# Optimization experiments

Measured on AMD Instinct MI355X. Metric: run time of the kernel, lower is better.

Reference implementation:

```python
import jax, jax.numpy as jnp
import numpy as np

N = 50000    # nodes
E = 600000   # edges
F = 128      # num_features
ED = 16      # edge_dim
H = 4        # heads
D = 32       # per-head channels = hidden_units // heads
HID = H * D  # hidden_units = 128
C = 10       # num_classes


def _lin(k, fan_in, fan_out):
    # torch.nn.Linear-style init scale
    return jax.random.uniform(k, (fan_in, fan_out), jnp.float32, -1.0, 1.0) / np.sqrt(fan_in)


def setup_inputs() -> dict:
    key = jax.random.key(0)
    ks = jax.random.split(key, 24)
    inp = {
        "x": jax.random.normal(ks[0], (N, F), jnp.float32),
        "edge_index": jax.random.randint(ks[1], (2, E), 0, N, dtype=jnp.int32),
        "edge_attr": jax.random.normal(ks[2], (E, ED), jnp.float32),
    }
    j = 3
    for l, ind in enumerate([F, HID]):
        specs = {"q": (ind, HID, True), "k": (ind, HID, True), "v": (ind, HID, True),
                 "e": (ED, HID, False), "s": (ind, HID, True)}
        for nm, (i, o, bias) in specs.items():
            inp[f"W{nm}{l}"] = _lin(ks[j], i, o); j += 1
            if bias:
                inp[f"b{nm}{l}"] = jnp.zeros((o,), jnp.float32)
    inp["Wout"] = _lin(ks[j], HID, C)
    inp["bout"] = jnp.zeros((C,), jnp.float32)
    return inp


def _transformer_conv(x, src, dst, eattr, Wq, bq, Wk, bk, Wv, bv, We, Ws, bs):
    # PyG TransformerConv: concat=True, root_weight=True, beta=False, eval dropout.
    n = x.shape[0]
    q = (x @ Wq + bq).reshape(n, H, D)
    k = (x @ Wk + bk).reshape(n, H, D)
    v = (x @ Wv + bv).reshape(n, H, D)
    e = (eattr @ We).reshape(-1, H, D)           # edge embedding, added to key and value
    kj = k[src] + e                              # [E, H, D]
    vj = v[src] + e                              # [E, H, D]
    logits = jnp.einsum("ehd,ehd->eh", q[dst], kj) / np.sqrt(D)
    m = jax.ops.segment_max(logits, dst, num_segments=n)          # [N, H]
    ex = jnp.exp(logits - m[dst])
    denom = jax.ops.segment_sum(ex, dst, num_segments=n)          # [N, H]
    alpha = ex / (denom[dst] + 1e-16)                             # PyG softmax eps
    out = jax.ops.segment_sum(vj * alpha[..., None], dst, num_segments=n)
    return out.reshape(n, HID) + x @ Ws + bs                      # concat heads + skip


def reference(x, edge_index, edge_attr,
              Wq0, bq0, Wk0, bk0, Wv0, bv0, We0, Ws0, bs0,
              Wq1, bq1, Wk1, bk1, Wv1, bv1, We1, Ws1, bs1,
              Wout, bout):
    src, dst = edge_index[0], edge_index[1]
    h = jax.nn.relu(_transformer_conv(x, src, dst, edge_attr,
                                      Wq0, bq0, Wk0, bk0, Wv0, bv0, We0, Ws0, bs0))
    h = jax.nn.relu(_transformer_conv(h, src, dst, edge_attr,
                                      Wq1, bq1, Wk1, bk1, Wv1, bv1, We1, Ws1, bs1))
    logits = h @ Wout + bout
    return jax.nn.log_softmax(logits, axis=1)
```

## Files before the change

### kernel.cpp

```cpp
#include <hip/hip_runtime.h>

typedef unsigned short u16;
typedef __attribute__((ext_vector_type(4))) u16 u16x4;
typedef __attribute__((ext_vector_type(8))) u16 u16x8;
typedef __attribute__((ext_vector_type(8))) short short8;
typedef __attribute__((ext_vector_type(4))) float f32x4;
typedef __attribute__((ext_vector_type(4))) float f4;

#define NN 50000
#define NE 600000
#define HEADS 4
#define DH 32
#define HIDU 128
#define NC 10
#define NBLK 196

__device__ __forceinline__ float bf2f(u16 u) {
    union { unsigned int i; float f; } c; c.i = ((unsigned int)u) << 16; return c.f;
}
__device__ __forceinline__ u16 f2bf(float f) {
    union { float f; unsigned int i; } c; c.f = f;
    unsigned int x = c.i;
    return (u16)((x + 0x7fffu + ((x >> 16) & 1u)) >> 16);
}

__global__ void k_zero(int* p, int n) {
    int i = blockIdx.x * blockDim.x + threadIdx.x;
    if (i < n) p[i] = 0;
}

__global__ void k_hist(const int* __restrict__ dst, int* __restrict__ deg) {
    int i = blockIdx.x * blockDim.x + threadIdx.x;
    if (i < NE) atomicAdd(&deg[dst[i]], 1);
}

__global__ __launch_bounds__(256) void scan_a(const int* __restrict__ deg,
                                              int* __restrict__ bsum) {
    __shared__ int red[4];
    int i = blockIdx.x * 256 + threadIdx.x;
    int v = (i < NN) ? deg[i] : 0;
    #pragma unroll
    for (int off = 1; off < 64; off <<= 1) v += __shfl_xor(v, off);
    if ((threadIdx.x & 63) == 0) red[threadIdx.x >> 6] = v;
    __syncthreads();
    if (threadIdx.x == 0) bsum[blockIdx.x] = red[0] + red[1] + red[2] + red[3];
}

__global__ __launch_bounds__(256) void scan_b(const int* __restrict__ bsum,
                                              int* __restrict__ boff,
                                              int* __restrict__ row_ptr) {
    __shared__ int s[256];
    int t = threadIdx.x;
    int v = (t < NBLK) ? bsum[t] : 0;
    s[t] = v;
    __syncthreads();
    for (int off = 1; off < 256; off <<= 1) {
        int x = (t >= off) ? s[t - off] : 0;
        __syncthreads();
        s[t] += x;
        __syncthreads();
    }
    if (t < NBLK) boff[t] = s[t] - v;
    if (t == 0) row_ptr[NN] = NE;
}

__global__ __launch_bounds__(256) void scan_c(const int* __restrict__ deg,
                                              const int* __restrict__ boff,
                                              int* __restrict__ row_ptr,
                                              int* __restrict__ cursor) {
    __shared__ int s[256];
    int t = threadIdx.x;
    int i = blockIdx.x * 256 + t;
    int v = (i < NN) ? deg[i] : 0;
    s[t] = v;
    __syncthreads();
    for (int off = 1; off < 256; off <<= 1) {
        int x = (t >= off) ? s[t - off] : 0;
        __syncthreads();
        s[t] += x;
        __syncthreads();
    }
    if (i < NN) {
        int r = boff[blockIdx.x] + s[t] - v;
        row_ptr[i] = r;
        cursor[i] = r;
    }
}

__global__ void k_scatter(const int* __restrict__ ei, const float* __restrict__ eattr,
                          int* __restrict__ cursor,
                          int* __restrict__ csr_src, u16* __restrict__ ea16) {
    int i = blockIdx.x * blockDim.x + threadIdx.x;
    if (i < NE) {
        int s = ei[i];
        int d = ei[NE + i];
        int pos = atomicAdd(&cursor[d], 1);
        csr_src[pos] = s;
        const f4* ep = (const f4*)(eattr + (size_t)i * 16);
        f4 a = ep[0], b = ep[1], c = ep[2], dd = ep[3];
        u16x8 o0, o1;
        #pragma unroll
        for (int j = 0; j < 4; j++) {
            o0[j] = f2bf(a[j]); o0[4 + j] = f2bf(b[j]);
            o1[j] = f2bf(c[j]); o1[4 + j] = f2bf(dd[j]);
        }
        *(u16x8*)(ea16 + (size_t)pos * 16)     = o0;
        *(u16x8*)(ea16 + (size_t)pos * 16 + 8) = o1;
    }
}

__global__ __launch_bounds__(256) void k_cvt(const float* __restrict__ in,
                                             u16* __restrict__ hi, u16* __restrict__ lo) {
    int i = blockIdx.x * 256 + threadIdx.x;
    const f4* p = (const f4*)(in + (size_t)i * 8);
    f4 a = p[0], b = p[1];
    float v[8] = {a[0], a[1], a[2], a[3], b[0], b[1], b[2], b[3]};
    u16x8 h, l;
    #pragma unroll
    for (int j = 0; j < 8; j++) {
        u16 hh = f2bf(v[j]);
        float r = v[j] - bf2f(hh);
        h[j] = hh; l[j] = f2bf(r);
    }
    *(u16x8*)(hi + (size_t)i * 8) = h;
    *(u16x8*)(lo + (size_t)i * 8) = l;
}

__global__ void k_cvtw(const float* w0, const float* w1, const float* w2, const float* w3,
                       const float* w4, const float* w5, const float* w6, const float* w7,
                       u16* __restrict__ hi, u16* __restrict__ lo) {
    const float* w;
    switch (blockIdx.x) {
        case 0: w = w0; break; case 1: w = w1; break;
        case 2: w = w2; break; case 3: w = w3; break;
        case 4: w = w4; break; case 5: w = w5; break;
        case 6: w = w6; break; default: w = w7; break;
    }
    u16* oh = hi + blockIdx.x * 16384;
    u16* ol = lo + blockIdx.x * 16384;
    for (int i = 0; i < 64; i++) {
        int idx = threadIdx.x + i * 256;
        int k = idx >> 7, n = idx & 127;
        float v = w[idx];
        u16 h = f2bf(v);
        float r = v - bf2f(h);
        oh[n * 128 + k] = h;
        ol[n * 128 + k] = f2bf(r);
    }
}

__global__ __launch_bounds__(256) void gemm_qkv(
    const u16* __restrict__ Xhi, const u16* __restrict__ WtHi,
    const float* __restrict__ b0, const float* __restrict__ b1,
    const float* __restrict__ b2,
    float* __restrict__ outq, u16* __restrict__ outk, u16* __restrict__ outv,
    int nrows)
{
    __shared__ u16 Bs[128 * 128];
    const int mat = blockIdx.y;
    const u16* wh = WtHi + mat * 16384;

    #pragma unroll
    for (int i = 0; i < 8; i++) {
        int idx = threadIdx.x + i * 256;
        int n = idx >> 4, g = idx & 15;
        Bs[0] = Bs[0];
        *(u16x8*)(&Bs[n * 128 + ((g ^ (n & 15)) << 3)]) = *(const u16x8*)(wh + n * 128 + g * 8);
    }
    __syncthreads();

    const int wave = threadIdx.x >> 6, lane = threadIdx.x & 63;
    const int n0 = lane & 15;
    const int qw = lane >> 4;
    const int kq = qw * 8;

    const u16* xh[2];
    #pragma unroll
    for (int rt = 0; rt < 2; rt++) {
        int arow = blockIdx.x * 128 + wave * 32 + rt * 16 + n0;
        int arow_c = arow < nrows ? arow : nrows - 1;
        xh[rt] = Xhi + (size_t)arow_c * HIDU + kq;
    }

    f32x4 acc[2][8];
    #pragma unroll
    for (int rt = 0; rt < 2; rt++)
        #pragma unroll
        for (int nt = 0; nt < 8; nt++) acc[rt][nt] = (f32x4){0.f, 0.f, 0.f, 0.f};

    #pragma unroll
    for (int ks = 0; ks < 4; ks++) {
        short8 ah[2];
        #pragma unroll
        for (int rt = 0; rt < 2; rt++) ah[rt] = *(const short8*)(xh[rt] + ks * 32);
        #pragma unroll
        for (int nt = 0; nt < 8; nt++) {
            const int boff = (nt * 16 + n0) * 128 + (((ks << 2) + qw) ^ n0) * 8;
            short8 bh = *(const short8*)(&Bs[boff]);
            #pragma unroll
            for (int rt = 0; rt < 2; rt++)
                acc[rt][nt] = __builtin_amdgcn_mfma_f32_16x16x32_bf16(ah[rt], bh, acc[rt][nt], 0, 0, 0);
        }
    }

    const float* bia = (mat == 0) ? b0 : (mat == 1) ? b1 : b2;
    #pragma unroll
    for (int rt = 0; rt < 2; rt++) {
        const int rbase = blockIdx.x * 128 + wave * 32 + rt * 16 + qw * 4;
        #pragma unroll
        for (int nt = 0; nt < 8; nt++) {
            int col = nt * 16 + n0;
            float bv = bia[col];
            #pragma unroll
            for (int r = 0; r < 4; r++) {
                int grow = rbase + r;
                if (grow < nrows) {
                    float v = acc[rt][nt][r] + bv;
                    if (mat == 0)      outq[(size_t)grow * HIDU + col] = v;
                    else if (mat == 1) outk[(size_t)grow * HIDU + col] = f2bf(v);
                    else               outv[(size_t)grow * HIDU + col] = f2bf(v);
                }
            }
        }
    }
}

__global__ __launch_bounds__(256) void gemm_s(
    const u16* __restrict__ Xhi, const u16* __restrict__ Xlo,
    const u16* __restrict__ wh, const u16* __restrict__ wl,
    const float* __restrict__ bia, float* __restrict__ outs, int nrows)
{
    __shared__ u16 Bs[2 * 128 * 128];

    #pragma unroll
    for (int i = 0; i < 8; i++) {
        int idx = threadIdx.x + i * 256;
        int n = idx >> 4, g = idx & 15;
        int dst = n * 128 + ((g ^ (n & 15)) << 3);
        *(u16x8*)(&Bs[dst])         = *(const u16x8*)(wh + n * 128 + g * 8);
        *(u16x8*)(&Bs[16384 + dst]) = *(const u16x8*)(wl + n * 128 + g * 8);
    }
    __syncthreads();

    const int wave = threadIdx.x >> 6, lane = threadIdx.x & 63;
    const int n0 = lane & 15;
    const int qw = lane >> 4;
    const int kq = qw * 8;

    const u16* xh[2]; const u16* xl[2];
    #pragma unroll
    for (int rt = 0; rt < 2; rt++) {
        int arow = blockIdx.x * 128 + wave * 32 + rt * 16 + n0;
        int arow_c = arow < nrows ? arow : nrows - 1;
        xh[rt] = Xhi + (size_t)arow_c * HIDU + kq;
        xl[rt] = Xlo + (size_t)arow_c * HIDU + kq;
    }

    f32x4 acc[2][8];
    #pragma unroll
    for (int rt = 0; rt < 2; rt++)
        #pragma unroll
        for (int nt = 0; nt < 8; nt++) acc[rt][nt] = (f32x4){0.f, 0.f, 0.f, 0.f};

    #pragma unroll
    for (int ks = 0; ks < 4; ks++) {
        short8 ah[2], al[2];
        #pragma unroll
        for (int rt = 0; rt < 2; rt++) {
            ah[rt] = *(const short8*)(xh[rt] + ks * 32);
            al[rt] = *(const short8*)(xl[rt] + ks * 32);
        }
        #pragma unroll
        for (int nt = 0; nt < 8; nt++) {
            const int boff = (nt * 16 + n0) * 128 + (((ks << 2) + qw) ^ n0) * 8;
            short8 bh = *(const short8*)(&Bs[boff]);
            short8 bl = *(const short8*)(&Bs[16384 + boff]);
            #pragma unroll
            for (int rt = 0; rt < 2; rt++) {
                acc[rt][nt] = __builtin_amdgcn_mfma_f32_16x16x32_bf16(ah[rt], bh, acc[rt][nt], 0, 0, 0);
                acc[rt][nt] = __builtin_amdgcn_mfma_f32_16x16x32_bf16(al[rt], bh, acc[rt][nt], 0, 0, 0);
                acc[rt][nt] = __builtin_amdgcn_mfma_f32_16x16x32_bf16(ah[rt], bl, acc[rt][nt], 0, 0, 0);
            }
        }
    }

    #pragma unroll
    for (int rt = 0; rt < 2; rt++) {
        const int rbase = blockIdx.x * 128 + wave * 32 + rt * 16 + qw * 4;
        #pragma unroll
        for (int nt = 0; nt < 8; nt++) {
            int col = nt * 16 + n0;
            float bv = bia[col];
            #pragma unroll
            for (int r = 0; r < 4; r++) {
                int grow = rbase + r;
                if (grow < nrows) outs[(size_t)grow * HIDU + col] = acc[rt][nt][r] + bv;
            }
        }
    }
}

__global__ __launch_bounds__(256) void attn(
    const float* __restrict__ qb, const u16* __restrict__ kb, const u16* __restrict__ vb,
    const float* __restrict__ sb, const u16* __restrict__ ea16, const float* __restrict__ We,
    const int* __restrict__ row_ptr, const int* __restrict__ csr_src,
    float* __restrict__ hout_f32, u16* __restrict__ hout_hi, u16* __restrict__ hout_lo,
    int mode)
{
    __shared__ float WeS[4 * 513];
    #pragma unroll
    for (int i = 0; i < 8; i++) {
        int idx = threadIdx.x + i * 256;
        int tt = idx >> 7, c = idx & 127;
        int h = c >> 5, j = c & 31;
        WeS[h * 513 + tt * 32 + j] = We[idx];
    }
    __syncthreads();

    int gtid = blockIdx.x * 256 + threadIdx.x;
    int n   = gtid >> 4;
    int l16 = gtid & 15;
    int h   = l16 >> 2;
    int sub = l16 & 3;
    const int lane = threadIdx.x & 63;
    const float* WeH = &WeS[h * 513];
    const int j0  = sub * 8;
    const int ch0 = h * DH + j0;
    const int t0  = sub * 4;

    float qreg[8];
    float g4[4];
    {
        const f4* qp = (const f4*)(qb + (size_t)n * HIDU + h * DH);
        float q32[32];
        #pragma unroll
        for (int c = 0; c < 8; c++) {
            f4 x = qp[c];
            #pragma unroll
            for (int j = 0; j < 4; j++) q32[c * 4 + j] = x[j];
        }
        #pragma unroll
        for (int tt = 0; tt < 4; tt++) {
            float a = 0.f;
            #pragma unroll
            for (int j = 0; j < 32; j++) a += q32[j] * WeH[(t0 + tt) * 32 + j];
            g4[tt] = a;
        }
        #pragma unroll
        for (int j = 0; j < 8; j++) qreg[j] = q32[j0 + j];
    }

    float m = -INFINITY, l = 0.f;
    float O[8];
    float a4[4];
    #pragma unroll
    for (int j = 0; j < 8; j++) O[j] = 0.f;
    #pragma unroll
    for (int tt = 0; tt < 4; tt++) a4[tt] = 0.f;

    const int r0 = row_ptr[n], r1 = row_ptr[n + 1];
    const float inv = 0.17677669529663687f;

    for (int e = r0; e < r1; e += 2) {
        bool has2 = (e + 1 < r1);
        int e1i = has2 ? e + 1 : e;
        int s0 = csr_src[e];
        int s1 = csr_src[e1i];
        u16x4 e0 = *(const u16x4*)(ea16 + (size_t)e * 16 + t0);
        u16x4 e1 = *(const u16x4*)(ea16 + (size_t)e1i * 16 + t0);

        u16x8 k0 = *(const u16x8*)(kb + (size_t)s0 * HIDU + ch0);
        u16x8 v0 = *(const u16x8*)(vb + (size_t)s0 * HIDU + ch0);
        u16x8 k1 = *(const u16x8*)(kb + (size_t)s1 * HIDU + ch0);
        u16x8 v1 = *(const u16x8*)(vb + (size_t)s1 * HIDU + ch0);

        float ea0[4], ea1[4];
        #pragma unroll
        for (int tt = 0; tt < 4; tt++) { ea0[tt] = bf2f(e0[tt]); ea1[tt] = bf2f(e1[tt]); }

        float d0 = 0.f, d1 = 0.f;
        #pragma unroll
        for (int j = 0; j < 8; j++) {
            d0 += qreg[j] * bf2f(k0[j]);
            d1 += qreg[j] * bf2f(k1[j]);
        }
        #pragma unroll
        for (int tt = 0; tt < 4; tt++) {
            d0 += g4[tt] * ea0[tt];
            d1 += g4[tt] * ea1[tt];
        }
        d0 += __shfl_xor(d0, 1);  d1 += __shfl_xor(d1, 1);
        d0 += __shfl_xor(d0, 2);  d1 += __shfl_xor(d1, 2);

        float logit0 = d0 * inv;
        float logit1 = has2 ? d1 * inv : -INFINITY;
        float mn = fmaxf(m, fmaxf(logit0, logit1));
        float corr = __expf(m - mn);
        float w0 = __expf(logit0 - mn);
        float w1 = __expf(logit1 - mn);
        l = l * corr + w0 + w1;
        #pragma unroll
        for (int j = 0; j < 8; j++)
            O[j] = O[j] * corr + w0 * bf2f(v0[j]) + w1 * bf2f(v1[j]);
        #pragma unroll
        for (int tt = 0; tt < 4; tt++)
            a4[tt] = a4[tt] * corr + w0 * ea0[tt] + w1 * ea1[tt];
        m = mn;
    }

    float af[16];
    #pragma unroll
    for (int t = 0; t < 16; t++)
        af[t] = __shfl(a4[t & 3], (lane & ~3) | (t >> 2));

    float invl = 1.0f / (l + 1e-16f);
    const float* sp = sb + (size_t)n * HIDU + ch0;
    const size_t obase = (size_t)n * HIDU + ch0;

    float vals[8];
    #pragma unroll
    for (int j = 0; j < 8; j++) {
        float ev = 0.f;
        #pragma unroll
        for (int t = 0; t < 16; t++) ev += af[t] * WeH[t * 32 + j0 + j];
        vals[j] = fmaxf((O[j] + ev) * invl + sp[j], 0.f);
    }
    if (mode == 0) {
        u16x8 hh, ll;
        #pragma unroll
        for (int j = 0; j < 8; j++) {
            u16 hv = f2bf(vals[j]);
            hh[j] = hv;
            ll[j] = f2bf(vals[j] - bf2f(hv));
        }
        *(u16x8*)(hout_hi + obase) = hh;
        *(u16x8*)(hout_lo + obase) = ll;
    } else {
        f4 r0v, r1v;
        #pragma unroll
        for (int j = 0; j < 4; j++) { r0v[j] = vals[j]; r1v[j] = vals[4 + j]; }
        *(f4*)(hout_f32 + obase) = r0v;
        *(f4*)(hout_f32 + obase + 4) = r1v;
    }
}

__global__ __launch_bounds__(256) void head_out(
    const float* __restrict__ hb, const float* __restrict__ Wout, const float* __restrict__ bout,
    float* __restrict__ out, int nnodes)
{
    __shared__ float Ws[HIDU * NC];
    __shared__ float bs[NC];
    for (int i = 0; i < 5; i++) {
        int idx = threadIdx.x + i * 256;
        if (idx < HIDU * NC) Ws[idx] = Wout[idx];
    }
    if (threadIdx.x < NC) bs[threadIdx.x] = bout[threadIdx.x];
    __syncthreads();

    int n = blockIdx.x * 256 + threadIdx.x;
    if (n >= nnodes) return;

    float lg[NC];
    #pragma unroll
    for (int c = 0; c < NC; c++) lg[c] = bs[c];
    const f4* hp = (const f4*)(hb + (size_t)n * HIDU);
    #pragma unroll
    for (int kc = 0; kc < 32; kc++) {
        f4 hv = hp[kc];
        #pragma unroll
        for (int j = 0; j < 4; j++) {
            float h = hv[j];
            int kk = kc * 4 + j;
            #pragma unroll
            for (int c = 0; c < NC; c++) lg[c] += h * Ws[kk * NC + c];
        }
    }
    float mx = lg[0];
    #pragma unroll
    for (int c = 1; c < NC; c++) mx = fmaxf(mx, lg[c]);
    float sum = 0.f;
    #pragma unroll
    for (int c = 0; c < NC; c++) sum += __expf(lg[c] - mx);
    float lse = mx + __logf(sum);
    #pragma unroll
    for (int c = 0; c < NC; c++) out[(size_t)n * NC + c] = lg[c] - lse;
}

extern "C" void kernel_launch(void* const* d_in, const int* in_sizes, int n_in,
                              void* d_out, int out_size, void* d_ws, size_t ws_size,
                              hipStream_t stream) {
    const float* x     = (const float*)d_in[0];
    const int*   ei    = (const int*)d_in[1];
    const float* eattr = (const float*)d_in[2];
    const float *Wq0 = (const float*)d_in[3],  *bq0 = (const float*)d_in[4];
    const float *Wk0 = (const float*)d_in[5],  *bk0 = (const float*)d_in[6];
    const float *Wv0 = (const float*)d_in[7],  *bv0 = (const float*)d_in[8];
    const float *We0 = (const float*)d_in[9];
    const float *Ws0 = (const float*)d_in[10], *bs0 = (const float*)d_in[11];
    const float *Wq1 = (const float*)d_in[12], *bq1 = (const float*)d_in[13];
    const float *Wk1 = (const float*)d_in[14], *bk1 = (const float*)d_in[15];
    const float *Wv1 = (const float*)d_in[16], *bv1 = (const float*)d_in[17];
    const float *We1 = (const float*)d_in[18];
    const float *Ws1 = (const float*)d_in[19], *bs1 = (const float*)d_in[20];
    const float *Wout = (const float*)d_in[21], *bout = (const float*)d_in[22];

    char* p = (char*)d_ws;
    auto alloc = [&](size_t bytes) -> void* {
        void* r = (void*)p;
        p += (bytes + 255) & ~(size_t)255;
        return r;
    };
    int* deg      = (int*)alloc(NN * 4);
    int* row_ptr  = (int*)alloc((NN + 1) * 4);
    int* cursor   = (int*)alloc(NN * 4);
    int* bsum     = (int*)alloc(NBLK * 4);
    int* boff     = (int*)alloc(NBLK * 4);
    int* csr_src  = (int*)alloc((size_t)NE * 4);
    float* qb     = (float*)alloc((size_t)NN * HIDU * 4);
    u16* kb       = (u16*)alloc((size_t)NN * HIDU * 2);
    u16* vb       = (u16*)alloc((size_t)NN * HIDU * 2);
    float* sbuf   = (float*)alloc((size_t)NN * HIDU * 4);
    float* hbuf   = (float*)alloc((size_t)NN * HIDU * 4);
    u16* ea16     = (u16*)alloc((size_t)NE * 16 * 2);
    u16* xhi      = (u16*)alloc((size_t)NN * HIDU * 2);
    u16* xlo      = (u16*)alloc((size_t)NN * HIDU * 2);
    u16* wthi     = (u16*)alloc(8 * 16384 * 2);
    u16* wtlo     = (u16*)alloc(8 * 16384 * 2);

    k_zero<<<(NN + 255) / 256, 256, 0, stream>>>(deg, NN);
    k_hist<<<(NE + 255) / 256, 256, 0, stream>>>(ei + NE, deg);
    scan_a<<<NBLK, 256, 0, stream>>>(deg, bsum);
    scan_b<<<1, 256, 0, stream>>>(bsum, boff, row_ptr);
    scan_c<<<NBLK, 256, 0, stream>>>(deg, boff, row_ptr, cursor);
    k_scatter<<<(NE + 255) / 256, 256, 0, stream>>>(ei, eattr, cursor, csr_src, ea16);

    k_cvtw<<<8, 256, 0, stream>>>(Wq0, Wk0, Wv0, Ws0, Wq1, Wk1, Wv1, Ws1, wthi, wtlo);

    const int gcv = (NN * HIDU / 8 + 255) / 256;
    const int gm = (NN + 127) / 128;
    const int ga = (NN * 16) / 256;

    k_cvt<<<gcv, 256, 0, stream>>>(x, xhi, xlo);
    gemm_qkv<<<dim3(gm, 3), 256, 0, stream>>>(xhi, wthi, bq0, bk0, bv0, qb, kb, vb, NN);
    gemm_s<<<gm, 256, 0, stream>>>(xhi, xlo, wthi + 3 * 16384, wtlo + 3 * 16384, bs0, sbuf, NN);
    attn<<<ga, 256, 0, stream>>>(qb, kb, vb, sbuf, ea16, We0,
                                 row_ptr, csr_src, hbuf, xhi, xlo, 0);
    gemm_qkv<<<dim3(gm, 3), 256, 0, stream>>>(xhi, wthi + 4 * 16384, bq1, bk1, bv1, qb, kb, vb, NN);
    gemm_s<<<gm, 256, 0, stream>>>(xhi, xlo, wthi + 7 * 16384, wtlo + 7 * 16384, bs1, sbuf, NN);
    attn<<<ga, 256, 0, stream>>>(qb, kb, vb, sbuf, ea16, We1,
                                 row_ptr, csr_src, hbuf, (u16*)nullptr, (u16*)nullptr, 1);
    head_out<<<(NN + 255) / 256, 256, 0, stream>>>(hbuf, Wout, bout, (float*)d_out, NN);
}
```

Measured before the change: 489.8 us.

## Fuse bf16 split into GEMMs, fuse output head into attention, use DPP reductions

Removes the standalone x-to-bf16 hi/lo conversion kernel and the bf16 hi/lo writes from layer-0 attention. The GEMMs now read fp32 activations directly and split them in registers, with the hi part taken by truncation instead of rounding. The separate head_out kernel is folded into layer-1 attention, which computes the 10-class logits and log-softmax per node through shared memory. Shuffle-xor reductions are replaced with DPP quad permutes. This saves launches and intermediate traffic, but the GEMMs read twice as many A bytes, truncation changes precision slightly, and attention gains more shared memory and a serial per-lane output dot product.

```diff
diff --git a/kernel.cpp b/kernel.cpp
--- a/kernel.cpp
+++ b/kernel.cpp
@@ -22,6 +22,14 @@
     union { float f; unsigned int i; } c; c.f = f;
     unsigned int x = c.i;
     return (u16)((x + 0x7fffu + ((x >> 16) & 1u)) >> 16);
+}
+__device__ __forceinline__ float qadd_xor1(float v) {
+    int o = __builtin_amdgcn_update_dpp(0, __float_as_int(v), 0xB1, 0xF, 0xF, true);
+    return v + __int_as_float(o);
+}
+__device__ __forceinline__ float qadd_xor2(float v) {
+    int o = __builtin_amdgcn_update_dpp(0, __float_as_int(v), 0x4E, 0xF, 0xF, true);
+    return v + __int_as_float(o);
 }
 
 __global__ void k_zero(int* p, int n) {
@@ -109,23 +117,6 @@
     }
 }
 
-__global__ __launch_bounds__(256) void k_cvt(const float* __restrict__ in,
-                                             u16* __restrict__ hi, u16* __restrict__ lo) {
-    int i = blockIdx.x * 256 + threadIdx.x;
-    const f4* p = (const f4*)(in + (size_t)i * 8);
-    f4 a = p[0], b = p[1];
-    float v[8] = {a[0], a[1], a[2], a[3], b[0], b[1], b[2], b[3]};
-    u16x8 h, l;
-    #pragma unroll
-    for (int j = 0; j < 8; j++) {
-        u16 hh = f2bf(v[j]);
-        float r = v[j] - bf2f(hh);
-        h[j] = hh; l[j] = f2bf(r);
-    }
-    *(u16x8*)(hi + (size_t)i * 8) = h;
-    *(u16x8*)(lo + (size_t)i * 8) = l;
-}
-
 __global__ void k_cvtw(const float* w0, const float* w1, const float* w2, const float* w3,
                        const float* w4, const float* w5, const float* w6, const float* w7,
                        u16* __restrict__ hi, u16* __restrict__ lo) {
@@ -150,7 +141,7 @@
 }
 
 __global__ __launch_bounds__(256) void gemm_qkv(
-    const u16* __restrict__ Xhi, const u16* __restrict__ WtHi,
+    const float* __restrict__ X, const u16* __restrict__ WtHi,
     const float* __restrict__ b0, const float* __restrict__ b1,
     const float* __restrict__ b2,
     float* __restrict__ outq, u16* __restrict__ outk, u16* __restrict__ outv,
@@ -164,7 +155,6 @@
     for (int i = 0; i < 8; i++) {
         int idx = threadIdx.x + i * 256;
         int n = idx >> 4, g = idx & 15;
-        Bs[0] = Bs[0];
         *(u16x8*)(&Bs[n * 128 + ((g ^ (n & 15)) << 3)]) = *(const u16x8*)(wh + n * 128 + g * 8);
     }
     __syncthreads();
@@ -174,12 +164,12 @@
     const int qw = lane >> 4;
     const int kq = qw * 8;
 
-    const u16* xh[2];
+    const float* xp[2];
     #pragma unroll
     for (int rt = 0; rt < 2; rt++) {
         int arow = blockIdx.x * 128 + wave * 32 + rt * 16 + n0;
         int arow_c = arow < nrows ? arow : nrows - 1;
-        xh[rt] = Xhi + (size_t)arow_c * HIDU + kq;
+        xp[rt] = X + (size_t)arow_c * HIDU + kq;
     }
 
     f32x4 acc[2][8];
@@ -192,7 +182,15 @@
     for (int ks = 0; ks < 4; ks++) {
         short8 ah[2];
         #pragma unroll
-        for (int rt = 0; rt < 2; rt++) ah[rt] = *(const short8*)(xh[rt] + ks * 32);
+        for (int rt = 0; rt < 2; rt++) {
+            f4 a0 = *(const f4*)(xp[rt] + ks * 32);
+            f4 a1 = *(const f4*)(xp[rt] + ks * 32 + 4);
+            #pragma unroll
+            for (int j = 0; j < 4; j++) {
+                ah[rt][j]     = (short)(__float_as_uint(a0[j]) >> 16);
+                ah[rt][4 + j] = (short)(__float_as_uint(a1[j]) >> 16);
+            }
+        }
         #pragma unroll
         for (int nt = 0; nt < 8; nt++) {
             const int boff = (nt * 16 + n0) * 128 + (((ks << 2) + qw) ^ n0) * 8;
@@ -226,7 +224,7 @@
 }
 
 __global__ __launch_bounds__(256) void gemm_s(
-    const u16* __restrict__ Xhi, const u16* __restrict__ Xlo,
+    const float* __restrict__ X,
     const u16* __restrict__ wh, const u16* __restrict__ wl,
     const float* __restrict__ bia, float* __restrict__ outs, int nrows)
 {
@@ -247,13 +245,12 @@
     const int qw = lane >> 4;
     const int kq = qw * 8;
 
-    const u16* xh[2]; const u16* xl[2];
+    const float* xp[2];
     #pragma unroll
     for (int rt = 0; rt < 2; rt++) {
         int arow = blockIdx.x * 128 + wave * 32 + rt * 16 + n0;
         int arow_c = arow < nrows ? arow : nrows - 1;
-        xh[rt] = Xhi + (size_t)arow_c * HIDU + kq;
-        xl[rt] = Xlo + (size_t)arow_c * HIDU + kq;
+        xp[rt] = X + (size_t)arow_c * HIDU + kq;
     }
 
     f32x4 acc[2][8];
@@ -267,8 +264,19 @@
         short8 ah[2], al[2];
         #pragma unroll
         for (int rt = 0; rt < 2; rt++) {
-            ah[rt] = *(const short8*)(xh[rt] + ks * 32);
-            al[rt] = *(const short8*)(xl[rt] + ks * 32);
+            f4 a0 = *(const f4*)(xp[rt] + ks * 32);
+            f4 a1 = *(const f4*)(xp[rt] + ks * 32 + 4);
+            #pragma unroll
+            for (int j = 0; j < 4; j++) {
+                unsigned u0 = __float_as_uint(a0[j]);
+                unsigned u1 = __float_as_uint(a1[j]);
+                ah[rt][j]     = (short)(u0 >> 16);
+                ah[rt][4 + j] = (short)(u1 >> 16);
+                float r0 = a0[j] - __uint_as_float(u0 & 0xffff0000u);
+                float r1 = a1[j] - __uint_as_float(u1 & 0xffff0000u);
+                al[rt][j]     = (short)(__float_as_uint(r0) >> 16);
+                al[rt][4 + j] = (short)(__float_as_uint(r1) >> 16);
+            }
         }
         #pragma unroll
         for (int nt = 0; nt < 8; nt++) {
@@ -304,16 +312,29 @@
     const float* __restrict__ qb, const u16* __restrict__ kb, const u16* __restrict__ vb,
     const float* __restrict__ sb, const u16* __restrict__ ea16, const float* __restrict__ We,
     const int* __restrict__ row_ptr, const int* __restrict__ csr_src,
-    float* __restrict__ hout_f32, u16* __restrict__ hout_hi, u16* __restrict__ hout_lo,
-    int mode)
+    float* __restrict__ hout_f32,
+    const float* __restrict__ Wout, const float* __restrict__ bout,
+    float* __restrict__ out_logits, int mode)
 {
     __shared__ float WeS[4 * 513];
+    __shared__ float WoS[HIDU * NC];
+    __shared__ float boS[NC];
+    __shared__ float hrowS[16 * 132];
+    __shared__ float lgS[16 * 16];
+
     #pragma unroll
     for (int i = 0; i < 8; i++) {
         int idx = threadIdx.x + i * 256;
         int tt = idx >> 7, c = idx & 127;
         int h = c >> 5, j = c & 31;
         WeS[h * 513 + tt * 32 + j] = We[idx];
+    }
+    if (mode == 1) {
+        for (int i = 0; i < 5; i++) {
+            int idx = threadIdx.x + i * 256;
+            if (idx < HIDU * NC) WoS[idx] = Wout[idx];
+        }
+        if (threadIdx.x < NC) boS[threadIdx.x] = bout[threadIdx.x];
     }
     __syncthreads();
 
@@ -389,8 +410,8 @@
             d0 += g4[tt] * ea0[tt];
             d1 += g4[tt] * ea1[tt];
         }
-        d0 += __shfl_xor(d0, 1);  d1 += __shfl_xor(d1, 1);
-        d0 += __shfl_xor(d0, 2);  d1 += __shfl_xor(d1, 2);
+        d0 = qadd_xor1(d0);  d1 = qadd_xor1(d1);
+        d0 = qadd_xor2(d0);  d1 = qadd_xor2(d1);
 
         float logit0 = d0 * inv;
         float logit1 = has2 ? d1 * inv : -INFINITY;
@@ -415,7 +436,6 @@
 
     float invl = 1.0f / (l + 1e-16f);
     const float* sp = sb + (size_t)n * HIDU + ch0;
-    const size_t obase = (size_t)n * HIDU + ch0;
 
     float vals[8];
     #pragma unroll
@@ -425,65 +445,43 @@
         for (int t = 0; t < 16; t++) ev += af[t] * WeH[t * 32 + j0 + j];
         vals[j] = fmaxf((O[j] + ev) * invl + sp[j], 0.f);
     }
+
     if (mode == 0) {
-        u16x8 hh, ll;
-        #pragma unroll
-        for (int j = 0; j < 8; j++) {
-            u16 hv = f2bf(vals[j]);
-            hh[j] = hv;
-            ll[j] = f2bf(vals[j] - bf2f(hv));
-        }
-        *(u16x8*)(hout_hi + obase) = hh;
-        *(u16x8*)(hout_lo + obase) = ll;
-    } else {
+        const size_t obase = (size_t)n * HIDU + ch0;
         f4 r0v, r1v;
         #pragma unroll
         for (int j = 0; j < 4; j++) { r0v[j] = vals[j]; r1v[j] = vals[4 + j]; }
         *(f4*)(hout_f32 + obase) = r0v;
         *(f4*)(hout_f32 + obase + 4) = r1v;
-    }
-}
-
-__global__ __launch_bounds__(256) void head_out(
-    const float* __restrict__ hb, const float* __restrict__ Wout, const float* __restrict__ bout,
-    float* __restrict__ out, int nnodes)
-{
-    __shared__ float Ws[HIDU * NC];
-    __shared__ float bs[NC];
-    for (int i = 0; i < 5; i++) {
-        int idx = threadIdx.x + i * 256;
-        if (idx < HIDU * NC) Ws[idx] = Wout[idx];
-    }
-    if (threadIdx.x < NC) bs[threadIdx.x] = bout[threadIdx.x];
-    __syncthreads();
-
-    int n = blockIdx.x * 256 + threadIdx.x;
-    if (n >= nnodes) return;
-
-    float lg[NC];
-    #pragma unroll
-    for (int c = 0; c < NC; c++) lg[c] = bs[c];
-    const f4* hp = (const f4*)(hb + (size_t)n * HIDU);
-    #pragma unroll
-    for (int kc = 0; kc < 32; kc++) {
-        f4 hv = hp[kc];
-        #pragma unroll
-        for (int j = 0; j < 4; j++) {
-            float h = hv[j];
-            int kk = kc * 4 + j;
-            #pragma unroll
-            for (int c = 0; c < NC; c++) lg[c] += h * Ws[kk * NC + c];
-        }
-    }
-    float mx = lg[0];
-    #pragma unroll
-    for (int c = 1; c < NC; c++) mx = fmaxf(mx, lg[c]);
-    float sum = 0.f;
-    #pragma unroll
-    for (int c = 0; c < NC; c++) sum += __expf(lg[c] - mx);
-    float lse = mx + __logf(sum);
-    #pragma unroll
-    for (int c = 0; c < NC; c++) out[(size_t)n * NC + c] = lg[c] - lse;
+    } else {
+        const int cb = threadIdx.x >> 4;
+        float* hr = &hrowS[cb * 132];
+        f4 w0v, w1v;
+        #pragma unroll
+        for (int j = 0; j < 4; j++) { w0v[j] = vals[j]; w1v[j] = vals[4 + j]; }
+        *(f4*)(hr + ch0) = w0v;
+        *(f4*)(hr + ch0 + 4) = w1v;
+        if (l16 < NC) {
+            float lg = boS[l16];
+            for (int ch = 0; ch < HIDU; ch += 4) {
+                f4 hv = *(const f4*)(hr + ch);
+                #pragma unroll
+                for (int j = 0; j < 4; j++) lg += hv[j] * WoS[(ch + j) * NC + l16];
+            }
+            lgS[cb * 16 + l16] = lg;
+        }
+        if (l16 < NC) {
+            float lgc = lgS[cb * 16 + l16];
+            float mx = -INFINITY;
+            #pragma unroll
+            for (int c = 0; c < NC; c++) mx = fmaxf(mx, lgS[cb * 16 + c]);
+            float sum = 0.f;
+            #pragma unroll
+            for (int c = 0; c < NC; c++) sum += __expf(lgS[cb * 16 + c] - mx);
+            float lse = mx + __logf(sum);
+            out_logits[(size_t)n * NC + l16] = lgc - lse;
+        }
+    }
 }
 
 extern "C" void kernel_launch(void* const* d_in, const int* in_sizes, int n_in,
@@ -522,8 +520,6 @@
     float* sbuf   = (float*)alloc((size_t)NN * HIDU * 4);
     float* hbuf   = (float*)alloc((size_t)NN * HIDU * 4);
     u16* ea16     = (u16*)alloc((size_t)NE * 16 * 2);
-    u16* xhi      = (u16*)alloc((size_t)NN * HIDU * 2);
-    u16* xlo      = (u16*)alloc((size_t)NN * HIDU * 2);
     u16* wthi     = (u16*)alloc(8 * 16384 * 2);
     u16* wtlo     = (u16*)alloc(8 * 16384 * 2);
 
@@ -536,18 +532,15 @@
 
     k_cvtw<<<8, 256, 0, stream>>>(Wq0, Wk0, Wv0, Ws0, Wq1, Wk1, Wv1, Ws1, wthi, wtlo);
 
-    const int gcv = (NN * HIDU / 8 + 255) / 256;
     const int gm = (NN + 127) / 128;
     const int ga = (NN * 16) / 256;
 
-    k_cvt<<<gcv, 256, 0, stream>>>(x, xhi, xlo);
-    gemm_qkv<<<dim3(gm, 3), 256, 0, stream>>>(xhi, wthi, bq0, bk0, bv0, qb, kb, vb, NN);
-    gemm_s<<<gm, 256, 0, stream>>>(xhi, xlo, wthi + 3 * 16384, wtlo + 3 * 16384, bs0, sbuf, NN);
-    attn<<<ga, 256, 0, stream>>>(qb, kb, vb, sbuf, ea16, We0,
-                                 row_ptr, csr_src, hbuf, xhi, xlo, 0);
-    gemm_qkv<<<dim3(gm, 3), 256, 0, stream>>>(xhi, wthi + 4 * 16384, bq1, bk1, bv1, qb, kb, vb, NN);
-    gemm_s<<<gm, 256, 0, stream>>>(xhi, xlo, wthi + 7 * 16384, wtlo + 7 * 16384, bs1, sbuf, NN);
-    attn<<<ga, 256, 0, stream>>>(qb, kb, vb, sbuf, ea16, We1,
-                                 row_ptr, csr_src, hbuf, (u16*)nullptr, (u16*)nullptr, 1);
-    head_out<<<(NN + 255) / 256, 256, 0, stream>>>(hbuf, Wout, bout, (float*)d_out, NN);
-}
+    gemm_qkv<<<dim3(gm, 3), 256, 0, stream>>>(x, wthi, bq0, bk0, bv0, qb, kb, vb, NN);
+    gemm_s<<<gm, 256, 0, stream>>>(x, wthi + 3 * 16384, wtlo + 3 * 16384, bs0, sbuf, NN);
+    attn<<<ga, 256, 0, stream>>>(qb, kb, vb, sbuf, ea16, We0, row_ptr, csr_src,
+                                 hbuf, Wout, bout, (float*)d_out, 0);
+    gemm_qkv<<<dim3(gm, 3), 256, 0, stream>>>(hbuf, wthi + 4 * 16384, bq1, bk1, bv1, qb, kb, vb, NN);
+    gemm_s<<<gm, 256, 0, stream>>>(hbuf, wthi + 7 * 16384, wtlo + 7 * 16384, bs1, sbuf, NN);
+    attn<<<ga, 256, 0, stream>>>(qb, kb, vb, sbuf, ea16, We1, row_ptr, csr_src,
+                                 hbuf, Wout, bout, (float*)d_out, 1);
+}
```

After: 469.2 us. 1.04x faster.
